# Performance work log

Measured on AMD Instinct MI355X. Metric: run time of the kernel, lower is better.

## Reference

```python
import jax, jax.numpy as jnp
import numpy as np
from jax import lax

# pywt db5 analysis filter bank (frozen buffers in the torch module)
DEC_LO = np.array([0.003335725285001549, -0.012580751999015526, -0.006241490213011705,
                   0.07757149384006515, -0.03224486958502952, -0.24229488706619015,
                   0.13842814590110342, 0.7243085284385744, 0.6038292697974729,
                   0.160102397974125], dtype=np.float32)
DEC_HI = np.array([-0.160102397974125, 0.6038292697974729, -0.7243085284385744,
                   0.13842814590110342, 0.24229488706619015, -0.03224486958502952,
                   -0.07757149384006515, -0.006241490213011705, 0.012580751999015526,
                   0.003335725285001549], dtype=np.float32)
NUM_LEVELS = 8  # min(round(log2(131072)), max_level=8)


def _conv1d(x, w, padding, lhs_dilation=(1,), groups=1):
    # x: [N, C, L], w: [O, I, K]; cross-correlation, matching torch F.conv1d
    return lax.conv_general_dilated(
        x, w, window_strides=(1,), padding=[padding], lhs_dilation=lhs_dilation,
        dimension_numbers=("NCH", "OIH", "NCH"), feature_group_count=groups)


def setup_inputs() -> dict:
    key = jax.random.key(0)
    k1, k2 = jax.random.split(key)
    x = jax.random.normal(k1, (128, 131072), dtype=jnp.float32)
    # small scale keeps the 8-level synthesis cascade numerically tame
    idwt_filters = jax.random.normal(k2, (128, 8, 2, 32), dtype=jnp.float32) * 0.05
    return {"x": x, "idwt_filters": idwt_filters}


def reference(x, idwt_filters):
    # x: [B, T]; idwt_filters: [B, levels, 2, kw] with kw even
    B, T = x.shape
    w_lo = jnp.asarray(DEC_LO).reshape(1, 1, -1)
    w_hi = jnp.asarray(DEC_HI).reshape(1, 1, -1)
    pad = DEC_LO.shape[0] // 2  # 5 -> conv output length L+1 for kernel 10

    # --- analysis DWT (frozen db5 filters), lengths: T/2^l + 1 per band ---
    lo = x[:, None, :]                       # [B,1,T]
    his = []
    for _ in range(NUM_LEVELS):
        y_lo = _conv1d(lo, w_lo, (pad, pad))
        y_hi = _conv1d(lo, w_hi, (pad, pad))
        lo = y_lo[:, :, ::2]
        his.append(y_hi[:, :, ::2])          # [B,1,T/2^l+1]

    # --- synthesis IDWT with predicted per-example filters (groups=B) ---
    kw = idwt_filters.shape[-1]
    p = kw // 2 - 1
    prev = jnp.transpose(lo, (1, 0, 2))      # [1,B,n]: batch as channels
    for i in range(NUM_LEVELS - 1, -1, -1):
        rec_lo = idwt_filters[:, i, 0, :][:, None, :]   # [B,1,kw]
        rec_hi = idwt_filters[:, i, 1, :][:, None, :]
        hi = jnp.transpose(his[i], (1, 0, 2))           # [1,B,n]
        # lhs_dilation=2 == zero-stuffing even indices; asym pad (p, p+1)
        # reproduces torch's trailing zero at index 2n-1; out length = 2n-1
        y_lo = _conv1d(prev, rec_lo, (p, p + 1), lhs_dilation=(2,), groups=B)
        y_hi = _conv1d(hi, rec_hi, (p, p + 1), lhs_dilation=(2,), groups=B)
        prev = y_lo + y_hi
    return prev[0, :, :-1]                   # [B, T]
```

## Files before the change

kernel.cpp:

```cpp
#include <hip/hip_runtime.h>


static __constant__ float c_dec_lo[10] = {
    0.003335725285001549f, -0.012580751999015526f, -0.006241490213011705f,
    0.07757149384006515f, -0.03224486958502952f, -0.24229488706619015f,
    0.13842814590110342f, 0.7243085284385744f, 0.6038292697974729f,
    0.160102397974125f};
static __constant__ float c_dec_hi[10] = {
    -0.160102397974125f, 0.6038292697974729f, -0.7243085284385744f,
    0.13842814590110342f, 0.24229488706619015f, -0.03224486958502952f,
    -0.07757149384006515f, -0.006241490213011705f, 0.012580751999015526f,
    0.003335725285001549f};

__device__ inline float4 ldz4(const float* __restrict__ row, int j, int L) {
  if (j >= 0 && j + 3 < L) return *reinterpret_cast<const float4*>(row + j);
  float4 r;
  r.x = (j + 0 >= 0 && j + 0 < L) ? row[j + 0] : 0.f;
  r.y = (j + 1 >= 0 && j + 1 < L) ? row[j + 1] : 0.f;
  r.z = (j + 2 >= 0 && j + 2 < L) ? row[j + 2] : 0.f;
  r.w = (j + 3 >= 0 && j + 3 < L) ? row[j + 3] : 0.f;
  return r;
}

__device__ inline void load20(const float* src, int base, float* v) {
#pragma unroll
  for (int q = 0; q < 5; ++q) {
    const float4 t = *reinterpret_cast<const float4*>(src + base + 4 * q);
    v[4 * q + 0] = t.x; v[4 * q + 1] = t.y;
    v[4 * q + 2] = t.z; v[4 * q + 3] = t.w;
  }
}

__device__ inline void fir10x2(const float* v, float* lo, float* hv) {
#pragma unroll
  for (int i = 0; i < 4; ++i) {
    float a = 0.f, h = 0.f;
#pragma unroll
    for (int k = 0; k < 10; ++k) {
      const float xx = v[2 * i + 3 + k];
      a += xx * c_dec_lo[k];
      h += xx * c_dec_hi[k];
    }
    lo[i] = a; hv[i] = h;
  }
}

__device__ inline void store_pad(float* S, int idx, const float* lo, int vlo,
                                 int vhi) {
  if (idx >= vlo && idx + 3 < vhi) {
    *reinterpret_cast<float4*>(S + idx) =
        make_float4(lo[0], lo[1], lo[2], lo[3]);
  } else {
#pragma unroll
    for (int i = 0; i < 4; ++i)
      S[idx + i] = (idx + i >= vlo && idx + i < vhi) ? lo[i] : 0.f;
  }
}

__device__ inline void store_hi(float* hg, int A, int idx, const float* hv,
                                int es, int ee) {
  if (idx >= es && idx + 3 < ee) {
    *reinterpret_cast<float4*>(hg + A + idx) =
        make_float4(hv[0], hv[1], hv[2], hv[3]);
  } else {
#pragma unroll
    for (int i = 0; i < 4; ++i)
      if (idx + i >= es && idx + i < ee) hg[A + idx + i] = hv[i];
  }
}

__global__ __launch_bounds__(512) void fwd03(
    const float* __restrict__ x, float* __restrict__ hi0,
    float* __restrict__ hi1, float* __restrict__ hi2,
    float* __restrict__ hi3, float* __restrict__ lo3) {
  const int b = blockIdx.y;
  const int b3 = blockIdx.x * 1024;
  __shared__ float S0[8276];
  __shared__ float S1[4132];
  const int tid = threadIdx.x;

  {
    const float* xr = x + (size_t)b * 131072;
    float* h0 = hi0 + (size_t)b * 65540;
    const int A0 = 8 * b3 - 56;
    const int vlo = -A0, vhi = 65537 - A0;
    const int ee = min(8248, vhi);
    const int xoff = 16 * b3 - 120;
    for (int idx = 4 * tid; idx < 8276; idx += 2048) {
      const int jb = 2 * idx + xoff;
      float v[20];
#pragma unroll
      for (int q = 0; q < 5; ++q) {
        const float4 t = ldz4(xr, jb + 4 * q, 131072);
        v[4 * q + 0] = t.x; v[4 * q + 1] = t.y;
        v[4 * q + 2] = t.z; v[4 * q + 3] = t.w;
      }
      float lo[4], hv[4];
      fir10x2(v, lo, hv);
      store_pad(S0, idx, lo, vlo, vhi);
      store_hi(h0, A0, idx, hv, 56, ee);
    }
  }
  __syncthreads();
  {
    float* h1 = hi1 + (size_t)b * 32772;
    const int A1 = 4 * b3 - 24;
    const int vlo = -A1, vhi = 32769 - A1;
    const int ee = min(4120, vhi);
    for (int idx = 4 * tid; idx < 4132; idx += 2048) {
      float v[20];
      load20(S0, 2 * idx, v);
      float lo[4], hv[4];
      fir10x2(v, lo, hv);
      store_pad(S1, idx, lo, vlo, vhi);
      store_hi(h1, A1, idx, hv, 24, ee);
    }
  }
  __syncthreads();
  {
    float* h2 = hi2 + (size_t)b * 16388;
    const int A2 = 2 * b3 - 8;
    const int vlo = -A2, vhi = 16385 - A2;
    const int ee = min(2056, vhi);
    for (int idx = 4 * tid; idx < 2060; idx += 2048) {
      float v[20];
      load20(S1, 2 * idx, v);
      float lo[4], hv[4];
      fir10x2(v, lo, hv);
      store_pad(S0, idx, lo, vlo, vhi);
      store_hi(h2, A2, idx, hv, 8, ee);
    }
  }
  __syncthreads();
  {
    float* l3 = lo3 + (size_t)b * 8196;
    float* h3 = hi3 + (size_t)b * 8196;
    const int ne3 = min(1024, 8193 - b3);
    for (int idx = 4 * tid; idx < 1024; idx += 2048) {
      float v[20];
      load20(S0, 2 * idx, v);
      float lo[4], hv[4];
      fir10x2(v, lo, hv);
      store_hi(l3, b3, idx, lo, 0, ne3);
      store_hi(h3, b3, idx, hv, 0, ne3);
    }
  }
}

__device__ inline void inv_accum(const float* p, const float* h,
                                 const float4* wpk, float* acc) {
#pragma unroll
  for (int i = 0; i < 8; ++i) acc[i] = 0.f;
#pragma unroll
  for (int m = 0; m < 16; ++m) {
    const float4 w = wpk[m];
#pragma unroll
    for (int e = 0; e < 4; ++e) {
      const float pe = p[e + 1 + m], he = h[e + 1 + m];
      acc[2 * e + 0] += pe * w.y + he * w.w;
      acc[2 * e + 1] += pe * w.x + he * w.z;
    }
  }
}

__device__ inline void inv_store_pad(float* S, int o, const float* acc,
                                     int vlo, int vhi) {
  if (o >= vlo && o + 7 < vhi) {
    *reinterpret_cast<float4*>(S + o) =
        make_float4(acc[0], acc[1], acc[2], acc[3]);
    *reinterpret_cast<float4*>(S + o + 4) =
        make_float4(acc[4], acc[5], acc[6], acc[7]);
  } else {
#pragma unroll
    for (int i = 0; i < 8; ++i)
      S[o + i] = (o + i >= vlo && o + i < vhi) ? acc[i] : 0.f;
  }
}

__device__ inline void inv_stage_lds(const float* Sprev, int reloff,
                                     const float* __restrict__ hig, int Dhi,
                                     int U0, float* Sout, int NOUT, int Aout,
                                     int lenOut, const float4* wpk, int tid) {
  const int vlo = -Aout, vhi = lenOut - Aout;
  for (int o = 8 * tid; o < NOUT; o += 4096) {
    const int rel = (o >> 1) + reloff;
    float p[20], h[20];
#pragma unroll
    for (int q = 0; q < 5; ++q) {
      const float4 a = *reinterpret_cast<const float4*>(Sprev + rel + 4 * q);
      p[4 * q + 0] = a.x; p[4 * q + 1] = a.y;
      p[4 * q + 2] = a.z; p[4 * q + 3] = a.w;
      const float4 bb = ldz4(hig, U0 + (o >> 1) + 4 * q, Dhi);
      h[4 * q + 0] = bb.x; h[4 * q + 1] = bb.y;
      h[4 * q + 2] = bb.z; h[4 * q + 3] = bb.w;
    }
    float acc[8];
    inv_accum(p, h, wpk, acc);
    inv_store_pad(Sout, o, acc, vlo, vhi);
  }
}

__device__ inline void inv_stage_glb(const float* __restrict__ pg, int Dp,
                                     int P0, const float* __restrict__ hig,
                                     int Dhi, int U0, float* Sout, int NOUT,
                                     int Aout, int lenOut, const float4* wpk,
                                     int tid) {
  const int vlo = -Aout, vhi = lenOut - Aout;
  for (int o = 8 * tid; o < NOUT; o += 4096) {
    float p[20], h[20];
#pragma unroll
    for (int q = 0; q < 5; ++q) {
      const float4 a = ldz4(pg, P0 + (o >> 1) + 4 * q, Dp);
      p[4 * q + 0] = a.x; p[4 * q + 1] = a.y;
      p[4 * q + 2] = a.z; p[4 * q + 3] = a.w;
      const float4 bb = ldz4(hig, U0 + (o >> 1) + 4 * q, Dhi);
      h[4 * q + 0] = bb.x; h[4 * q + 1] = bb.y;
      h[4 * q + 2] = bb.z; h[4 * q + 3] = bb.w;
    }
    float acc[8];
    inv_accum(p, h, wpk, acc);
    inv_store_pad(Sout, o, acc, vlo, vhi);
  }
}

__device__ inline void inv_stage_out(const float* Sprev,
                                     const float* __restrict__ hig, int Dhi,
                                     int U0, float* __restrict__ og,
                                     const float4* wpk, int tid) {
  for (int o = 8 * tid; o < 16384; o += 4096) {
    const int rel = o >> 1;
    float p[20], h[20];
#pragma unroll
    for (int q = 0; q < 5; ++q) {
      const float4 a = *reinterpret_cast<const float4*>(Sprev + rel + 4 * q);
      p[4 * q + 0] = a.x; p[4 * q + 1] = a.y;
      p[4 * q + 2] = a.z; p[4 * q + 3] = a.w;
      const float4 bb = ldz4(hig, U0 + (o >> 1) + 4 * q, Dhi);
      h[4 * q + 0] = bb.x; h[4 * q + 1] = bb.y;
      h[4 * q + 2] = bb.z; h[4 * q + 3] = bb.w;
    }
    float acc[8];
    inv_accum(p, h, wpk, acc);
    *reinterpret_cast<float4*>(og + o) =
        make_float4(acc[0], acc[1], acc[2], acc[3]);
    *reinterpret_cast<float4*>(og + o + 4) =
        make_float4(acc[4], acc[5], acc[6], acc[7]);
  }
}

__global__ __launch_bounds__(512) void inv03(
    const float* __restrict__ prev3, const float* __restrict__ hi3,
    const float* __restrict__ hi2, const float* __restrict__ hi1,
    const float* __restrict__ hi0, const float* __restrict__ filt,
    float* __restrict__ out) {
  const int c = blockIdx.y;
  const int t0b = blockIdx.x * 16384;
  __shared__ float X[8208];
  __shared__ float Y[4128];
  __shared__ float4 wp[64];
  const int tid = threadIdx.x;
  if (tid < 64) {
    const int lvl = tid >> 4, m = tid & 15;
    const float* f = filt + ((size_t)c * 8 + (3 - lvl)) * 64;
    wp[tid] = make_float4(f[2 * m], f[2 * m + 1], f[32 + 2 * m],
                          f[32 + 2 * m + 1]);
  }
  __syncthreads();
  const float* p3 = prev3 + (size_t)c * 8196;
  const float* h3 = hi3 + (size_t)c * 8196;
  const float* h2 = hi2 + (size_t)c * 16388;
  const float* h1 = hi1 + (size_t)c * 32772;
  const float* h0 = hi0 + (size_t)c * 65540;
  inv_stage_glb(p3, 8193, t0b / 16 - 16, h3, 8193, t0b / 16 - 16, X, 2080,
                t0b / 8 - 16, 16385, wp, tid);
  __syncthreads();
  inv_stage_lds(X, 0, h2, 16385, t0b / 8 - 16, Y, 4128, t0b / 4 - 16, 32769,
                wp + 16, tid);
  __syncthreads();
  inv_stage_lds(Y, 4, h1, 32769, t0b / 4 - 12, X, 8208, t0b / 2 - 8, 65537,
                wp + 32, tid);
  __syncthreads();
  inv_stage_out(X, h0, 65537, t0b / 2 - 8, out + (size_t)c * 131072 + t0b,
                wp + 48, tid);
}

__device__ inline void fwd_tail_level(const float* __restrict__ in,
                                      float* __restrict__ outp, int L, int D,
                                      float* __restrict__ hirow, int tid) {
  for (int d0 = 4 * tid; d0 < D; d0 += 2048) {
    const int jb = 2 * d0 - 8;
    float v[20];
    const bool interior = (jb >= 0) && (jb + 19 < L) && (d0 + 3 < D);
    if (interior) {
#pragma unroll
      for (int q = 0; q < 5; ++q) {
        const float4 t = *reinterpret_cast<const float4*>(in + jb + 4 * q);
        v[4 * q + 0] = t.x; v[4 * q + 1] = t.y;
        v[4 * q + 2] = t.z; v[4 * q + 3] = t.w;
      }
    } else {
#pragma unroll
      for (int q = 0; q < 20; ++q) {
        const int j = jb + q;
        v[q] = (j >= 0 && j < L) ? in[j] : 0.f;
      }
    }
    float lo[4], hv[4];
    fir10x2(v, lo, hv);
    if (interior) {
      *reinterpret_cast<float4*>(outp + d0) =
          make_float4(lo[0], lo[1], lo[2], lo[3]);
      *reinterpret_cast<float4*>(hirow + d0) =
          make_float4(hv[0], hv[1], hv[2], hv[3]);
    } else {
#pragma unroll
      for (int i = 0; i < 4; ++i)
        if (d0 + i < D) { outp[d0 + i] = lo[i]; hirow[d0 + i] = hv[i]; }
    }
  }
}

__device__ inline void inv_tail_level(const float* __restrict__ pin,
                                      float* __restrict__ pout, int L,
                                      const float* __restrict__ hirow,
                                      const float* __restrict__ filt, int c,
                                      int level, int tid, float4* wpack) {
  __syncthreads();
  if (tid < 16) {
    const float* f = filt + ((size_t)c * 8 + level) * 64;
    wpack[tid] = make_float4(f[2 * tid], f[2 * tid + 1], f[32 + 2 * tid],
                             f[32 + 2 * tid + 1]);
  }
  __syncthreads();
  const int Tout = 2 * L - 1;
  for (int t0 = 8 * tid; t0 < Tout; t0 += 4096) {
    const int U = t0 / 2 - 8;
    float p[20], h[20];
    if (U >= 0 && U + 19 < L) {
#pragma unroll
      for (int q = 0; q < 5; ++q) {
        const float4 a = *reinterpret_cast<const float4*>(pin + U + 4 * q);
        p[4 * q + 0] = a.x; p[4 * q + 1] = a.y;
        p[4 * q + 2] = a.z; p[4 * q + 3] = a.w;
        const float4 bb = *reinterpret_cast<const float4*>(hirow + U + 4 * q);
        h[4 * q + 0] = bb.x; h[4 * q + 1] = bb.y;
        h[4 * q + 2] = bb.z; h[4 * q + 3] = bb.w;
      }
    } else {
#pragma unroll
      for (int q = 0; q < 20; ++q) {
        const int j = U + q;
        p[q] = (j >= 0 && j < L) ? pin[j] : 0.f;
        h[q] = (j >= 0 && j < L) ? hirow[j] : 0.f;
      }
    }
    float acc[8];
    inv_accum(p, h, wpack, acc);
    if (t0 + 7 < Tout) {
      *reinterpret_cast<float4*>(pout + t0) =
          make_float4(acc[0], acc[1], acc[2], acc[3]);
      *reinterpret_cast<float4*>(pout + t0 + 4) =
          make_float4(acc[4], acc[5], acc[6], acc[7]);
    } else {
#pragma unroll
      for (int i = 0; i < 8; ++i)
        if (t0 + i < Tout) pout[t0 + i] = acc[i];
    }
  }
}

__global__ __launch_bounds__(512) void mid_fused(
    const float* __restrict__ lo3, const float* __restrict__ filt,
    float* __restrict__ prev3out) {
  const int b = blockIdx.x;
  __shared__ float A[8200];
  __shared__ float Bb[4104];
  __shared__ float H4[4100];
  __shared__ float H5[2052];
  __shared__ float H6[1028];
  __shared__ float H7[516];
  __shared__ float4 wpack[16];
  const int tid = threadIdx.x;
  const float* row = lo3 + (size_t)b * 8196;
  for (int j4 = tid; j4 < 2048; j4 += 512)
    *reinterpret_cast<float4*>(A + 4 * j4) =
        *reinterpret_cast<const float4*>(row + 4 * j4);
  if (tid == 0) A[8192] = row[8192];
  __syncthreads();
  fwd_tail_level(A, Bb, 8193, 4097, H4, tid);
  __syncthreads();
  fwd_tail_level(Bb, A, 4097, 2049, H5, tid);
  __syncthreads();
  fwd_tail_level(A, Bb, 2049, 1025, H6, tid);
  __syncthreads();
  fwd_tail_level(Bb, A, 1025, 513, H7, tid);
  inv_tail_level(A, Bb, 513, H7, filt, b, 7, tid, wpack);
  inv_tail_level(Bb, A, 1025, H6, filt, b, 6, tid, wpack);
  inv_tail_level(A, Bb, 2049, H5, filt, b, 5, tid, wpack);
  inv_tail_level(Bb, prev3out + (size_t)b * 8196, 4097, H4, filt, b, 4, tid,
                 wpack);
}

extern "C" void kernel_launch(void* const* d_in, const int* in_sizes, int n_in,
                              void* d_out, int out_size, void* d_ws,
                              size_t ws_size, hipStream_t stream) {
  const float* x = (const float*)d_in[0];
  const float* filt = (const float*)d_in[1];
  float* out = (float*)d_out;
  float* ws = (float*)d_ws;

  const int B = 128;
  float* lo3buf = ws;
  float* prev3buf = lo3buf + (size_t)B * 8196;
  float* hi0 = prev3buf + (size_t)B * 8196;
  float* hi1 = hi0 + (size_t)B * 65540;
  float* hi2 = hi1 + (size_t)B * 32772;
  float* hi3 = hi2 + (size_t)B * 16388;

  hipLaunchKernelGGL(fwd03, dim3(9, B), dim3(512), 0, stream, x, hi0, hi1, hi2,
                     hi3, lo3buf);
  hipLaunchKernelGGL(mid_fused, dim3(B), dim3(512), 0, stream, lo3buf, filt,
                     prev3buf);
  hipLaunchKernelGGL(inv03, dim3(8, B), dim3(512), 0, stream, prev3buf, hi3,
                     hi2, hi1, hi0, filt, out);
}
```

Baseline: 153.4 us.

## Halve fused DWT tile size and add boundary-free fast path for interior tiles

The forward (fwd03) and inverse (inv03) fused multi-level kernels now use tiles half as wide with 256-thread blocks, doubling the grid (17 and 16 blocks per row). Interior tiles take a templated fast path that uses unconditional float4 loads and stores with no zero-padding checks. Edge tiles keep the bounds-checked path. Smaller tiles raise occupancy and parallelism and cut LDS per block, at the cost of more halo recomputation relative to useful work.

```diff
diff --git a/kernel.cpp b/kernel.cpp
--- a/kernel.cpp
+++ b/kernel.cpp
@@ -31,6 +31,16 @@
   }
 }
 
+__device__ inline void load20z(const float* __restrict__ src, int base, int L,
+                               float* v) {
+#pragma unroll
+  for (int q = 0; q < 5; ++q) {
+    const float4 t = ldz4(src, base + 4 * q, L);
+    v[4 * q + 0] = t.x; v[4 * q + 1] = t.y;
+    v[4 * q + 2] = t.z; v[4 * q + 3] = t.w;
+  }
+}
+
 __device__ inline void fir10x2(const float* v, float* lo, float* hv) {
 #pragma unroll
   for (int i = 0; i < 4; ++i) {
@@ -69,80 +79,100 @@
   }
 }
 
-__global__ __launch_bounds__(512) void fwd03(
+__device__ inline void st4(float* dst, const float* a) {
+  *reinterpret_cast<float4*>(dst) = make_float4(a[0], a[1], a[2], a[3]);
+}
+
+__global__ __launch_bounds__(256) void fwd03(
     const float* __restrict__ x, float* __restrict__ hi0,
     float* __restrict__ hi1, float* __restrict__ hi2,
     float* __restrict__ hi3, float* __restrict__ lo3) {
   const int b = blockIdx.y;
-  const int b3 = blockIdx.x * 1024;
-  __shared__ float S0[8276];
-  __shared__ float S1[4132];
+  const int bx = blockIdx.x;
+  const int b3 = bx * 512;
+  __shared__ float S0[4180];
+  __shared__ float S1[2084];
   const int tid = threadIdx.x;
-
-  {
-    const float* xr = x + (size_t)b * 131072;
-    float* h0 = hi0 + (size_t)b * 65540;
-    const int A0 = 8 * b3 - 56;
-    const int vlo = -A0, vhi = 65537 - A0;
-    const int ee = min(8248, vhi);
-    const int xoff = 16 * b3 - 120;
-    for (int idx = 4 * tid; idx < 8276; idx += 2048) {
-      const int jb = 2 * idx + xoff;
-      float v[20];
-#pragma unroll
-      for (int q = 0; q < 5; ++q) {
-        const float4 t = ldz4(xr, jb + 4 * q, 131072);
-        v[4 * q + 0] = t.x; v[4 * q + 1] = t.y;
-        v[4 * q + 2] = t.z; v[4 * q + 3] = t.w;
-      }
-      float lo[4], hv[4];
-      fir10x2(v, lo, hv);
-      store_pad(S0, idx, lo, vlo, vhi);
-      store_hi(h0, A0, idx, hv, 56, ee);
-    }
-  }
-  __syncthreads();
-  {
-    float* h1 = hi1 + (size_t)b * 32772;
-    const int A1 = 4 * b3 - 24;
-    const int vlo = -A1, vhi = 32769 - A1;
-    const int ee = min(4120, vhi);
-    for (int idx = 4 * tid; idx < 4132; idx += 2048) {
-      float v[20];
-      load20(S0, 2 * idx, v);
-      float lo[4], hv[4];
-      fir10x2(v, lo, hv);
-      store_pad(S1, idx, lo, vlo, vhi);
-      store_hi(h1, A1, idx, hv, 24, ee);
-    }
-  }
-  __syncthreads();
-  {
-    float* h2 = hi2 + (size_t)b * 16388;
-    const int A2 = 2 * b3 - 8;
-    const int vlo = -A2, vhi = 16385 - A2;
-    const int ee = min(2056, vhi);
-    for (int idx = 4 * tid; idx < 2060; idx += 2048) {
-      float v[20];
-      load20(S1, 2 * idx, v);
-      float lo[4], hv[4];
-      fir10x2(v, lo, hv);
-      store_pad(S0, idx, lo, vlo, vhi);
-      store_hi(h2, A2, idx, hv, 8, ee);
-    }
-  }
-  __syncthreads();
-  {
-    float* l3 = lo3 + (size_t)b * 8196;
-    float* h3 = hi3 + (size_t)b * 8196;
-    const int ne3 = min(1024, 8193 - b3);
-    for (int idx = 4 * tid; idx < 1024; idx += 2048) {
-      float v[20];
-      load20(S0, 2 * idx, v);
-      float lo[4], hv[4];
-      fir10x2(v, lo, hv);
-      store_hi(l3, b3, idx, lo, 0, ne3);
-      store_hi(h3, b3, idx, hv, 0, ne3);
+  const bool fast = (bx >= 1) && (bx <= 14);
+  const float* xr = x + (size_t)b * 131072;
+  float* h0 = hi0 + (size_t)b * 65540;
+  float* h1 = hi1 + (size_t)b * 32772;
+  float* h2 = hi2 + (size_t)b * 16388;
+  float* h3 = hi3 + (size_t)b * 8196;
+  float* l3 = lo3 + (size_t)b * 8196;
+  const int A0 = 8 * b3 - 56, A1 = 4 * b3 - 24, A2 = 2 * b3 - 8;
+  const int xoff = 2 * A0 - 8;
+
+  if (fast) {
+    for (int idx = 4 * tid; idx < 4180; idx += 1024) {
+      float v[20]; load20(xr, 2 * idx + xoff, v);
+      float lo[4], hv[4]; fir10x2(v, lo, hv);
+      st4(S0 + idx, lo);
+      if (idx >= 56 && idx < 4152) st4(h0 + A0 + idx, hv);
+    }
+    __syncthreads();
+    for (int idx = 4 * tid; idx < 2084; idx += 1024) {
+      float v[20]; load20(S0, 2 * idx, v);
+      float lo[4], hv[4]; fir10x2(v, lo, hv);
+      st4(S1 + idx, lo);
+      if (idx >= 24 && idx < 2072) st4(h1 + A1 + idx, hv);
+    }
+    __syncthreads();
+    for (int idx = 4 * tid; idx < 1036; idx += 1024) {
+      float v[20]; load20(S1, 2 * idx, v);
+      float lo[4], hv[4]; fir10x2(v, lo, hv);
+      st4(S0 + idx, lo);
+      if (idx >= 8 && idx < 1032) st4(h2 + A2 + idx, hv);
+    }
+    __syncthreads();
+    for (int idx = 4 * tid; idx < 512; idx += 1024) {
+      float v[20]; load20(S0, 2 * idx, v);
+      float lo[4], hv[4]; fir10x2(v, lo, hv);
+      st4(l3 + b3 + idx, lo);
+      st4(h3 + b3 + idx, hv);
+    }
+  } else {
+    {
+      const int vlo = -A0, vhi = 65537 - A0;
+      const int ee = min(4152, vhi);
+      for (int idx = 4 * tid; idx < 4180; idx += 1024) {
+        float v[20]; load20z(xr, 2 * idx + xoff, 131072, v);
+        float lo[4], hv[4]; fir10x2(v, lo, hv);
+        store_pad(S0, idx, lo, vlo, vhi);
+        store_hi(h0, A0, idx, hv, 56, ee);
+      }
+    }
+    __syncthreads();
+    {
+      const int vlo = -A1, vhi = 32769 - A1;
+      const int ee = min(2072, vhi);
+      for (int idx = 4 * tid; idx < 2084; idx += 1024) {
+        float v[20]; load20(S0, 2 * idx, v);
+        float lo[4], hv[4]; fir10x2(v, lo, hv);
+        store_pad(S1, idx, lo, vlo, vhi);
+        store_hi(h1, A1, idx, hv, 24, ee);
+      }
+    }
+    __syncthreads();
+    {
+      const int vlo = -A2, vhi = 16385 - A2;
+      const int ee = min(1032, vhi);
+      for (int idx = 4 * tid; idx < 1036; idx += 1024) {
+        float v[20]; load20(S1, 2 * idx, v);
+        float lo[4], hv[4]; fir10x2(v, lo, hv);
+        store_pad(S0, idx, lo, vlo, vhi);
+        store_hi(h2, A2, idx, hv, 8, ee);
+      }
+    }
+    __syncthreads();
+    {
+      const int ne3 = min(512, 8193 - b3);
+      for (int idx = 4 * tid; idx < 512; idx += 1024) {
+        float v[20]; load20(S0, 2 * idx, v);
+        float lo[4], hv[4]; fir10x2(v, lo, hv);
+        store_hi(l3, b3, idx, lo, 0, ne3);
+        store_hi(h3, b3, idx, hv, 0, ne3);
+      }
     }
   }
 }
@@ -166,10 +196,8 @@
 __device__ inline void inv_store_pad(float* S, int o, const float* acc,
                                      int vlo, int vhi) {
   if (o >= vlo && o + 7 < vhi) {
-    *reinterpret_cast<float4*>(S + o) =
-        make_float4(acc[0], acc[1], acc[2], acc[3]);
-    *reinterpret_cast<float4*>(S + o + 4) =
-        make_float4(acc[4], acc[5], acc[6], acc[7]);
+    st4(S + o, acc);
+    st4(S + o + 4, acc + 4);
   } else {
 #pragma unroll
     for (int i = 0; i < 8; ++i)
@@ -177,86 +205,84 @@
   }
 }
 
-__device__ inline void inv_stage_lds(const float* Sprev, int reloff,
-                                     const float* __restrict__ hig, int Dhi,
-                                     int U0, float* Sout, int NOUT, int Aout,
-                                     int lenOut, const float4* wpk, int tid) {
+template <bool FAST>
+__device__ inline void inv_stage_g(const float* __restrict__ pg,
+                                   const float* __restrict__ hig, int Dp,
+                                   int P0, float* Sout, int NOUT, int Aout,
+                                   int lenOut, const float4* wpk, int tid) {
   const int vlo = -Aout, vhi = lenOut - Aout;
-  for (int o = 8 * tid; o < NOUT; o += 4096) {
-    const int rel = (o >> 1) + reloff;
+  for (int o = 8 * tid; o < NOUT; o += 2048) {
+    const int uh = o >> 1;
     float p[20], h[20];
-#pragma unroll
-    for (int q = 0; q < 5; ++q) {
-      const float4 a = *reinterpret_cast<const float4*>(Sprev + rel + 4 * q);
-      p[4 * q + 0] = a.x; p[4 * q + 1] = a.y;
-      p[4 * q + 2] = a.z; p[4 * q + 3] = a.w;
-      const float4 bb = ldz4(hig, U0 + (o >> 1) + 4 * q, Dhi);
-      h[4 * q + 0] = bb.x; h[4 * q + 1] = bb.y;
-      h[4 * q + 2] = bb.z; h[4 * q + 3] = bb.w;
+    if (FAST) {
+      load20(pg, P0 + uh, p);
+      load20(hig, P0 + uh, h);
+    } else {
+      load20z(pg, P0 + uh, Dp, p);
+      load20z(hig, P0 + uh, Dp, h);
     }
     float acc[8];
     inv_accum(p, h, wpk, acc);
-    inv_store_pad(Sout, o, acc, vlo, vhi);
-  }
-}
-
-__device__ inline void inv_stage_glb(const float* __restrict__ pg, int Dp,
-                                     int P0, const float* __restrict__ hig,
-                                     int Dhi, int U0, float* Sout, int NOUT,
-                                     int Aout, int lenOut, const float4* wpk,
-                                     int tid) {
+    if (FAST) {
+      st4(Sout + o, acc);
+      st4(Sout + o + 4, acc + 4);
+    } else {
+      inv_store_pad(Sout, o, acc, vlo, vhi);
+    }
+  }
+}
+
+template <bool FAST>
+__device__ inline void inv_stage_l(const float* Sprev, int reloff,
+                                   const float* __restrict__ hig, int Dhi,
+                                   int U0, float* Sout, int NOUT, int Aout,
+                                   int lenOut, const float4* wpk, int tid) {
   const int vlo = -Aout, vhi = lenOut - Aout;
-  for (int o = 8 * tid; o < NOUT; o += 4096) {
+  for (int o = 8 * tid; o < NOUT; o += 2048) {
+    const int uh = o >> 1;
     float p[20], h[20];
-#pragma unroll
-    for (int q = 0; q < 5; ++q) {
-      const float4 a = ldz4(pg, P0 + (o >> 1) + 4 * q, Dp);
-      p[4 * q + 0] = a.x; p[4 * q + 1] = a.y;
-      p[4 * q + 2] = a.z; p[4 * q + 3] = a.w;
-      const float4 bb = ldz4(hig, U0 + (o >> 1) + 4 * q, Dhi);
-      h[4 * q + 0] = bb.x; h[4 * q + 1] = bb.y;
-      h[4 * q + 2] = bb.z; h[4 * q + 3] = bb.w;
-    }
+    load20(Sprev, uh + reloff, p);
+    if (FAST) load20(hig, U0 + uh, h);
+    else load20z(hig, U0 + uh, Dhi, h);
     float acc[8];
     inv_accum(p, h, wpk, acc);
-    inv_store_pad(Sout, o, acc, vlo, vhi);
-  }
-}
-
-__device__ inline void inv_stage_out(const float* Sprev,
-                                     const float* __restrict__ hig, int Dhi,
-                                     int U0, float* __restrict__ og,
-                                     const float4* wpk, int tid) {
-  for (int o = 8 * tid; o < 16384; o += 4096) {
-    const int rel = o >> 1;
+    if (FAST) {
+      st4(Sout + o, acc);
+      st4(Sout + o + 4, acc + 4);
+    } else {
+      inv_store_pad(Sout, o, acc, vlo, vhi);
+    }
+  }
+}
+
+template <bool FAST>
+__device__ inline void inv_stage_o(const float* Sprev,
+                                   const float* __restrict__ hig, int Dhi,
+                                   int U0, float* __restrict__ og,
+                                   const float4* wpk, int tid) {
+  for (int o = 8 * tid; o < 8192; o += 2048) {
+    const int uh = o >> 1;
     float p[20], h[20];
-#pragma unroll
-    for (int q = 0; q < 5; ++q) {
-      const float4 a = *reinterpret_cast<const float4*>(Sprev + rel + 4 * q);
-      p[4 * q + 0] = a.x; p[4 * q + 1] = a.y;
-      p[4 * q + 2] = a.z; p[4 * q + 3] = a.w;
-      const float4 bb = ldz4(hig, U0 + (o >> 1) + 4 * q, Dhi);
-      h[4 * q + 0] = bb.x; h[4 * q + 1] = bb.y;
-      h[4 * q + 2] = bb.z; h[4 * q + 3] = bb.w;
-    }
+    load20(Sprev, uh, p);
+    if (FAST) load20(hig, U0 + uh, h);
+    else load20z(hig, U0 + uh, Dhi, h);
     float acc[8];
     inv_accum(p, h, wpk, acc);
-    *reinterpret_cast<float4*>(og + o) =
-        make_float4(acc[0], acc[1], acc[2], acc[3]);
-    *reinterpret_cast<float4*>(og + o + 4) =
-        make_float4(acc[4], acc[5], acc[6], acc[7]);
-  }
-}
-
-__global__ __launch_bounds__(512) void inv03(
+    st4(og + o, acc);
+    st4(og + o + 4, acc + 4);
+  }
+}
+
+__global__ __launch_bounds__(256) void inv03(
     const float* __restrict__ prev3, const float* __restrict__ hi3,
     const float* __restrict__ hi2, const float* __restrict__ hi1,
     const float* __restrict__ hi0, const float* __restrict__ filt,
     float* __restrict__ out) {
   const int c = blockIdx.y;
-  const int t0b = blockIdx.x * 16384;
-  __shared__ float X[8208];
-  __shared__ float Y[4128];
+  const int bx = blockIdx.x;
+  const int t0b = bx * 8192;
+  __shared__ float X[4112];
+  __shared__ float Y[2080];
   __shared__ float4 wp[64];
   const int tid = threadIdx.x;
   if (tid < 64) {
@@ -266,22 +292,37 @@
                           f[32 + 2 * m + 1]);
   }
   __syncthreads();
+  const bool fast = (bx >= 1) && (bx <= 14);
   const float* p3 = prev3 + (size_t)c * 8196;
   const float* h3 = hi3 + (size_t)c * 8196;
   const float* h2 = hi2 + (size_t)c * 16388;
   const float* h1 = hi1 + (size_t)c * 32772;
   const float* h0 = hi0 + (size_t)c * 65540;
-  inv_stage_glb(p3, 8193, t0b / 16 - 16, h3, 8193, t0b / 16 - 16, X, 2080,
-                t0b / 8 - 16, 16385, wp, tid);
-  __syncthreads();
-  inv_stage_lds(X, 0, h2, 16385, t0b / 8 - 16, Y, 4128, t0b / 4 - 16, 32769,
-                wp + 16, tid);
-  __syncthreads();
-  inv_stage_lds(Y, 4, h1, 32769, t0b / 4 - 12, X, 8208, t0b / 2 - 8, 65537,
-                wp + 32, tid);
-  __syncthreads();
-  inv_stage_out(X, h0, 65537, t0b / 2 - 8, out + (size_t)c * 131072 + t0b,
-                wp + 48, tid);
+  float* og = out + (size_t)c * 131072 + t0b;
+
+  if (fast) {
+    inv_stage_g<true>(p3, h3, 8193, t0b / 16 - 16, X, 1056, t0b / 8 - 16,
+                      16385, wp, tid);
+    __syncthreads();
+    inv_stage_l<true>(X, 0, h2, 16385, t0b / 8 - 16, Y, 2080, t0b / 4 - 16,
+                      32769, wp + 16, tid);
+    __syncthreads();
+    inv_stage_l<true>(Y, 4, h1, 32769, t0b / 4 - 12, X, 4112, t0b / 2 - 8,
+                      65537, wp + 32, tid);
+    __syncthreads();
+    inv_stage_o<true>(X, h0, 65537, t0b / 2 - 8, og, wp + 48, tid);
+  } else {
+    inv_stage_g<false>(p3, h3, 8193, t0b / 16 - 16, X, 1056, t0b / 8 - 16,
+                       16385, wp, tid);
+    __syncthreads();
+    inv_stage_l<false>(X, 0, h2, 16385, t0b / 8 - 16, Y, 2080, t0b / 4 - 16,
+                       32769, wp + 16, tid);
+    __syncthreads();
+    inv_stage_l<false>(Y, 4, h1, 32769, t0b / 4 - 12, X, 4112, t0b / 2 - 8,
+                       65537, wp + 32, tid);
+    __syncthreads();
+    inv_stage_o<false>(X, h0, 65537, t0b / 2 - 8, og, wp + 48, tid);
+  }
 }
 
 __device__ inline void fwd_tail_level(const float* __restrict__ in,
@@ -292,12 +333,7 @@
     float v[20];
     const bool interior = (jb >= 0) && (jb + 19 < L) && (d0 + 3 < D);
     if (interior) {
-#pragma unroll
-      for (int q = 0; q < 5; ++q) {
-        const float4 t = *reinterpret_cast<const float4*>(in + jb + 4 * q);
-        v[4 * q + 0] = t.x; v[4 * q + 1] = t.y;
-        v[4 * q + 2] = t.z; v[4 * q + 3] = t.w;
-      }
+      load20(in, jb, v);
     } else {
 #pragma unroll
       for (int q = 0; q < 20; ++q) {
@@ -308,10 +344,8 @@
     float lo[4], hv[4];
     fir10x2(v, lo, hv);
     if (interior) {
-      *reinterpret_cast<float4*>(outp + d0) =
-          make_float4(lo[0], lo[1], lo[2], lo[3]);
-      *reinterpret_cast<float4*>(hirow + d0) =
-          make_float4(hv[0], hv[1], hv[2], hv[3]);
+      st4(outp + d0, lo);
+      st4(hirow + d0, hv);
     } else {
 #pragma unroll
       for (int i = 0; i < 4; ++i)
@@ -337,15 +371,8 @@
     const int U = t0 / 2 - 8;
     float p[20], h[20];
     if (U >= 0 && U + 19 < L) {
-#pragma unroll
-      for (int q = 0; q < 5; ++q) {
-        const float4 a = *reinterpret_cast<const float4*>(pin + U + 4 * q);
-        p[4 * q + 0] = a.x; p[4 * q + 1] = a.y;
-        p[4 * q + 2] = a.z; p[4 * q + 3] = a.w;
-        const float4 bb = *reinterpret_cast<const float4*>(hirow + U + 4 * q);
-        h[4 * q + 0] = bb.x; h[4 * q + 1] = bb.y;
-        h[4 * q + 2] = bb.z; h[4 * q + 3] = bb.w;
-      }
+      load20(pin, U, p);
+      load20(hirow, U, h);
     } else {
 #pragma unroll
       for (int q = 0; q < 20; ++q) {
@@ -357,10 +384,8 @@
     float acc[8];
     inv_accum(p, h, wpack, acc);
     if (t0 + 7 < Tout) {
-      *reinterpret_cast<float4*>(pout + t0) =
-          make_float4(acc[0], acc[1], acc[2], acc[3]);
-      *reinterpret_cast<float4*>(pout + t0 + 4) =
-          make_float4(acc[4], acc[5], acc[6], acc[7]);
+      st4(pout + t0, acc);
+      st4(pout + t0 + 4, acc + 4);
     } else {
 #pragma unroll
       for (int i = 0; i < 8; ++i)
@@ -417,10 +442,10 @@
   float* hi2 = hi1 + (size_t)B * 32772;
   float* hi3 = hi2 + (size_t)B * 16388;
 
-  hipLaunchKernelGGL(fwd03, dim3(9, B), dim3(512), 0, stream, x, hi0, hi1, hi2,
-                     hi3, lo3buf);
+  hipLaunchKernelGGL(fwd03, dim3(17, B), dim3(256), 0, stream, x, hi0, hi1,
+                     hi2, hi3, lo3buf);
   hipLaunchKernelGGL(mid_fused, dim3(B), dim3(512), 0, stream, lo3buf, filt,
                      prev3buf);
-  hipLaunchKernelGGL(inv03, dim3(8, B), dim3(512), 0, stream, prev3buf, hi3,
+  hipLaunchKernelGGL(inv03, dim3(16, B), dim3(256), 0, stream, prev3buf, hi3,
                      hi2, hi1, hi0, filt, out);
 }
```

After: 149.7 us. 1.02x faster.
